# Optimization experiments

Hardware: AMD Instinct MI355X
Metric: run time of the kernel (lower is better)

The kernel has to match this reference:

```python
import jax, jax.numpy as jnp
import numpy as np

N_NODES = 50000


def _sage_conv(x, src, dst, Wl, Wr, bl, num_nodes):
    # PyG SAGEConv (mean aggr): out = lin_l(mean_{j in N(i)} x_j) + lin_r(x_i)
    # messages flow src -> dst
    agg = jax.ops.segment_sum(x[src], dst, num_segments=num_nodes)          # [N, F]
    deg = jax.ops.segment_sum(jnp.ones_like(dst, dtype=x.dtype), dst,
                              num_segments=num_nodes)                       # [N]
    agg = agg / jnp.maximum(deg, 1.0)[:, None]
    return agg @ Wl + bl + x @ Wr


def setup_inputs() -> dict:
    key = jax.random.key(0)
    ks = jax.random.split(key, 9)
    F_in, H, C, E = 256, 256, 40, 800000
    s = lambda fan: 1.0 / np.sqrt(fan)
    x = jax.random.normal(ks[0], (N_NODES, F_in), dtype=jnp.float32)
    edge_index = jax.random.randint(ks[1], (2, E), 0, N_NODES, dtype=jnp.int32)
    W1l = jax.random.normal(ks[2], (F_in, H), dtype=jnp.float32) * s(F_in)
    W1r = jax.random.normal(ks[3], (F_in, H), dtype=jnp.float32) * s(F_in)
    b1 = jnp.zeros((H,), dtype=jnp.float32)
    W2l = jax.random.normal(ks[4], (H, C), dtype=jnp.float32) * s(H)
    W2r = jax.random.normal(ks[5], (H, C), dtype=jnp.float32) * s(H)
    b2 = jnp.zeros((C,), dtype=jnp.float32)
    Q = jax.random.normal(ks[6], (E // 2, C), dtype=jnp.float32) * s(E // 2)
    return {"x": x, "edge_index": edge_index, "W1l": W1l, "b1": b1,
            "W1r": W1r, "W2l": W2l, "b2": b2, "W2r": W2r, "Q": Q}


def reference(x, edge_index, W1l, b1, W1r, W2l, b2, W2r, Q):
    # Eval mode: F.dropout with training=False is identity.
    src, dst = edge_index[0], edge_index[1]
    h = _sage_conv(x, src, dst, W1l, W1r, b1, N_NODES)
    h = jax.nn.elu(h)
    out = _sage_conv(h, src, dst, W2l, W2r, b2, N_NODES)
    return (out, Q)
```

## Files before the change

kernel.cpp:

```cpp
#include <hip/hip_runtime.h>
#include <hip/hip_bf16.h>
#include <cstddef>

#define N_NODES 50000
#define M_PAD 50048

typedef __attribute__((ext_vector_type(8))) short short8;
typedef __attribute__((ext_vector_type(4))) float floatx4;

__device__ inline unsigned short f2bf(float f) {
    union { float f; unsigned u; } v; v.f = f;
    unsigned r = v.u + 0x7fff + ((v.u >> 16) & 1);
    return (unsigned short)(r >> 16);
}
__device__ inline float bf2f(unsigned short s) {
    union { unsigned u; float f; } v; v.u = ((unsigned)s) << 16; return v.f;
}
__device__ inline float bfbits_lo(unsigned u) {
    union { unsigned u; float f; } v; v.u = u << 16; return v.f;
}
__device__ inline float bfbits_hi(unsigned u) {
    union { unsigned u; float f; } v; v.u = u & 0xffff0000u; return v.f;
}

__device__ inline void gload16(const void* g, void* l) {
    __builtin_amdgcn_global_load_lds(
        (const __attribute__((address_space(1))) unsigned int*)g,
        (__attribute__((address_space(3))) unsigned int*)l, 16, 0, 0);
}


__global__ void count_kernel(const int* __restrict__ dst, int* __restrict__ deg, int E) {
    for (int e = blockIdx.x * blockDim.x + threadIdx.x; e < E; e += gridDim.x * blockDim.x)
        atomicAdd(&deg[dst[e]], 1);
}

__global__ __launch_bounds__(256) void scan1_kernel(const int* __restrict__ deg,
                                                    int* __restrict__ blocksums, int n) {
    __shared__ int s[256];
    int t = threadIdx.x;
    int i = blockIdx.x * 256 + t;
    s[t] = (i < n) ? deg[i] : 0;
    __syncthreads();
    for (int off = 128; off > 0; off >>= 1) {
        if (t < off) s[t] += s[t + off];
        __syncthreads();
    }
    if (t == 0) blocksums[blockIdx.x] = s[0];
}

__global__ __launch_bounds__(256) void scan2_kernel(const int* __restrict__ blocksums,
                                                    int* __restrict__ blockoff, int nb) {
    __shared__ int s[256];
    int t = threadIdx.x;
    s[t] = (t < nb) ? blocksums[t] : 0;
    __syncthreads();
    for (int off = 1; off < 256; off <<= 1) {
        int u = (t >= off) ? s[t - off] : 0;
        __syncthreads();
        s[t] += u;
        __syncthreads();
    }
    if (t < nb) blockoff[t] = (t == 0) ? 0 : s[t - 1];
}

__global__ __launch_bounds__(256) void scan3_kernel(const int* __restrict__ deg,
                                                    const int* __restrict__ blockoff,
                                                    int* __restrict__ rowptr,
                                                    float* __restrict__ inv_deg,
                                                    int n, int E) {
    __shared__ int s[256];
    int t = threadIdx.x;
    int i = blockIdx.x * 256 + t;
    int v = (i < n) ? deg[i] : 0;
    s[t] = v;
    __syncthreads();
    for (int off = 1; off < 256; off <<= 1) {
        int u = (t >= off) ? s[t - off] : 0;
        __syncthreads();
        s[t] += u;
        __syncthreads();
    }
    if (i < n) {
        rowptr[i] = s[t] - v + blockoff[blockIdx.x];
        inv_deg[i] = 1.0f / (float)(v > 1 ? v : 1);
    }
    if (blockIdx.x == 0 && t == 0) rowptr[n] = E;
}

__global__ void fill_kernel(const int* __restrict__ src, const int* __restrict__ dst,
                            const int* __restrict__ rowptr, int* __restrict__ cnt,
                            int* __restrict__ csr, int E) {
    for (int e = blockIdx.x * blockDim.x + threadIdx.x; e < E; e += gridDim.x * blockDim.x) {
        int d = dst[e];
        int p = rowptr[d] + atomicAdd(&cnt[d], 1);
        csr[p] = src[e];
    }
}

__global__ __launch_bounds__(256) void prep_kernel(
    const float* __restrict__ x,
    const float* __restrict__ W1l, const float* __restrict__ W1r,
    const float* __restrict__ W2l, const float* __restrict__ W2r,
    unsigned short* __restrict__ Abuf, unsigned short* __restrict__ B1t,
    unsigned short* __restrict__ B2t) {
    int b = blockIdx.x;
    int tid = threadIdx.x;
    if (b < 6250) {
        int i = b * 256 + tid;
        int row = i >> 5;
        int c8 = i & 31;
        const float4* xp = reinterpret_cast<const float4*>(x + (size_t)row * 256 + c8 * 8);
        float4 v0 = xp[0], v1 = xp[1];
        uint4 o;
        o.x = (unsigned)f2bf(v0.x) | ((unsigned)f2bf(v0.y) << 16);
        o.y = (unsigned)f2bf(v0.z) | ((unsigned)f2bf(v0.w) << 16);
        o.z = (unsigned)f2bf(v1.x) | ((unsigned)f2bf(v1.y) << 16);
        o.w = (unsigned)f2bf(v1.z) | ((unsigned)f2bf(v1.w) << 16);
        *reinterpret_cast<uint4*>(Abuf + (size_t)row * 512 + 256 + c8 * 8) = o;
    } else if (b < 6250 + 512) {
        int idx = (b - 6250) * 256 + tid;
        int n = idx >> 9, k = idx & 511;
        float v = (k < 256) ? W1l[(size_t)k * 256 + n] : W1r[(size_t)(k - 256) * 256 + n];
        B1t[(size_t)n * 512 + k] = f2bf(v);
    } else {
        int idx = (b - 6250 - 512) * 256 + tid;
        int n = idx >> 8, k = idx & 255;
        float v = (n < 40) ? W2l[(size_t)k * 40 + n] : W2r[(size_t)k * 40 + (n - 40)];
        B2t[(size_t)n * 256 + k] = f2bf(v);
    }
}

__global__ __launch_bounds__(256) void aggregate1_q(
    const unsigned short* __restrict__ Abuf, const int* __restrict__ rowptr,
    const int* __restrict__ csr, const float* __restrict__ inv_deg,
    unsigned short* __restrict__ AbufOut, int N, int nAggBlocks,
    const float4* __restrict__ Qsrc, float4* __restrict__ Qdst, int nQ4) {
    if ((int)blockIdx.x >= nAggBlocks) {
        int idx = (blockIdx.x - nAggBlocks) * 256 + threadIdx.x;
        int stride = (gridDim.x - nAggBlocks) * 256;
        for (int i = idx; i < nQ4; i += stride) Qdst[i] = Qsrc[i];
        return;
    }
    int wv = blockIdx.x * 4 + (threadIdx.x >> 6);
    int node = wv * 2 + ((threadIdx.x >> 5) & 1);
    if (node >= N) return;
    int lane = threadIdx.x & 31;
    float a0 = 0.f, a1 = 0.f, a2 = 0.f, a3 = 0.f;
    float a4 = 0.f, a5 = 0.f, a6 = 0.f, a7 = 0.f;
    int beg = rowptr[node], end = rowptr[node + 1];
    int k = beg;
    for (; k + 4 <= end; k += 4) {
        uint4 v[4];
        #pragma unroll
        for (int u = 0; u < 4; ++u) {
            int j = csr[k + u];
            v[u] = *reinterpret_cast<const uint4*>(Abuf + (size_t)j * 512 + 256 + lane * 8);
        }
        #pragma unroll
        for (int u = 0; u < 4; ++u) {
            a0 += bfbits_lo(v[u].x); a1 += bfbits_hi(v[u].x);
            a2 += bfbits_lo(v[u].y); a3 += bfbits_hi(v[u].y);
            a4 += bfbits_lo(v[u].z); a5 += bfbits_hi(v[u].z);
            a6 += bfbits_lo(v[u].w); a7 += bfbits_hi(v[u].w);
        }
    }
    for (; k < end; ++k) {
        int j = csr[k];
        uint4 v = *reinterpret_cast<const uint4*>(Abuf + (size_t)j * 512 + 256 + lane * 8);
        a0 += bfbits_lo(v.x); a1 += bfbits_hi(v.x);
        a2 += bfbits_lo(v.y); a3 += bfbits_hi(v.y);
        a4 += bfbits_lo(v.z); a5 += bfbits_hi(v.z);
        a6 += bfbits_lo(v.w); a7 += bfbits_hi(v.w);
    }
    float s = inv_deg[node];
    uint4 w;
    w.x = (unsigned)f2bf(a0 * s) | ((unsigned)f2bf(a1 * s) << 16);
    w.y = (unsigned)f2bf(a2 * s) | ((unsigned)f2bf(a3 * s) << 16);
    w.z = (unsigned)f2bf(a4 * s) | ((unsigned)f2bf(a5 * s) << 16);
    w.w = (unsigned)f2bf(a6 * s) | ((unsigned)f2bf(a7 * s) << 16);
    *reinterpret_cast<uint4*>(AbufOut + (size_t)node * 512 + lane * 8) = w;
}

__global__ __launch_bounds__(256) void gemm1_mfma(
    const unsigned short* __restrict__ Abuf,
    const unsigned short* __restrict__ B1t,
    const float* __restrict__ bias,
    unsigned short* __restrict__ H,
    int M) {
    __shared__ unsigned short As[2][64 * 64];
    __shared__ unsigned short Bs[2][128 * 64];
    int tid = threadIdx.x;
    int row0 = blockIdx.x * 64;
    int bn = blockIdx.y;
    int wid = tid >> 6, lane = tid & 63;
    int wm = (wid >> 1) * 32;
    int wn = (wid & 1) * 64;
    int fr = lane & 15, fq = lane >> 4;

    int lrow8 = lane >> 3;
    int gco = ((lane & 7) ^ lrow8) * 8;
    const unsigned short* gA0 = Abuf + (size_t)(row0 + wid * 16 + 0 + lrow8) * 512 + gco;
    const unsigned short* gA1 = Abuf + (size_t)(row0 + wid * 16 + 8 + lrow8) * 512 + gco;
    const unsigned short* gB0 = B1t + (size_t)(bn * 128 + wid * 32 + 0  + lrow8) * 512 + gco;
    const unsigned short* gB1 = B1t + (size_t)(bn * 128 + wid * 32 + 8  + lrow8) * 512 + gco;
    const unsigned short* gB2 = B1t + (size_t)(bn * 128 + wid * 32 + 16 + lrow8) * 512 + gco;
    const unsigned short* gB3 = B1t + (size_t)(bn * 128 + wid * 32 + 24 + lrow8) * 512 + gco;

    floatx4 acc[2][4] = {};

    #define STAGE(buf, k0)                                       \
        gload16(gA0 + (k0), &As[buf][(wid * 16 + 0) * 64]);      \
        gload16(gA1 + (k0), &As[buf][(wid * 16 + 8) * 64]);      \
        gload16(gB0 + (k0), &Bs[buf][(wid * 32 + 0) * 64]);      \
        gload16(gB1 + (k0), &Bs[buf][(wid * 32 + 8) * 64]);      \
        gload16(gB2 + (k0), &Bs[buf][(wid * 32 + 16) * 64]);     \
        gload16(gB3 + (k0), &Bs[buf][(wid * 32 + 24) * 64]);

    #define COMPUTE(buf)                                                                  \
        {                                                                                 \
            _Pragma("unroll")                                                             \
            for (int kc = 0; kc < 2; ++kc) {                                              \
                short8 af[2], bfr[4];                                                     \
                _Pragma("unroll")                                                         \
                for (int mi = 0; mi < 2; ++mi) {                                          \
                    int row = wm + mi * 16 + fr;                                          \
                    af[mi] = *reinterpret_cast<const short8*>(                            \
                        &As[buf][row * 64 + (((kc * 4 + fq) ^ (fr & 7)) * 8)]);           \
                }                                                                         \
                _Pragma("unroll")                                                         \
                for (int ni = 0; ni < 4; ++ni) {                                          \
                    int row = wn + ni * 16 + fr;                                          \
                    bfr[ni] = *reinterpret_cast<const short8*>(                           \
                        &Bs[buf][row * 64 + (((kc * 4 + fq) ^ (fr & 7)) * 8)]);           \
                }                                                                         \
                _Pragma("unroll")                                                         \
                for (int mi = 0; mi < 2; ++mi)                                            \
                    _Pragma("unroll")                                                     \
                    for (int ni = 0; ni < 4; ++ni)                                        \
                        acc[mi][ni] = __builtin_amdgcn_mfma_f32_16x16x32_bf16(            \
                            af[mi], bfr[ni], acc[mi][ni], 0, 0, 0);                       \
            }                                                                             \
        }

    STAGE(0, 0);
    __syncthreads();
    int cur = 0;
    #pragma unroll 1
    for (int t = 0; t < 7; ++t) {
        STAGE(cur ^ 1, (t + 1) * 64);
        COMPUTE(cur);
        __syncthreads();
        cur ^= 1;
    }
    COMPUTE(cur);
    #undef STAGE
    #undef COMPUTE

    #pragma unroll
    for (int ni = 0; ni < 4; ++ni) {
        int gcol = bn * 128 + wn + ni * 16 + fr;
        float bb = bias[gcol];
        #pragma unroll
        for (int mi = 0; mi < 2; ++mi) {
            #pragma unroll
            for (int r = 0; r < 4; ++r) {
                int grow = row0 + wm + mi * 16 + fq * 4 + r;
                float t = acc[mi][ni][r] + bb;
                t = (t > 0.f) ? t : expm1f(t);
                H[(size_t)grow * 256 + gcol] = f2bf(t);
            }
        }
    }
}

__global__ __launch_bounds__(256) void gemm2_mfma(
    const unsigned short* __restrict__ Hb,
    const unsigned short* __restrict__ B2t,
    const float* __restrict__ b2,
    unsigned short* __restrict__ Plb,
    float* __restrict__ Pr,
    int M) {
    __shared__ unsigned short Bsm[80 * 256];
    __shared__ unsigned short As[2][64 * 64];
    int tid = threadIdx.x;
    int row0 = blockIdx.x * 64;
    int wid = tid >> 6, lane = tid & 63;
    int wm = wid * 16;
    int fr = lane & 15, fq = lane >> 4;

    for (int c = tid; c < 2560; c += 256) {
        int n = c >> 5, ci = c & 31;
        short8 v = *reinterpret_cast<const short8*>(B2t + (size_t)n * 256 + ci * 8);
        *reinterpret_cast<short8*>(&Bsm[n * 256 + ((ci ^ (n & 7)) * 8)]) = v;
    }

    int lrow8 = lane >> 3;
    int gco = ((lane & 7) ^ lrow8) * 8;
    const unsigned short* gA0 = Hb + (size_t)(row0 + wid * 16 + 0 + lrow8) * 256 + gco;
    const unsigned short* gA1 = Hb + (size_t)(row0 + wid * 16 + 8 + lrow8) * 256 + gco;

    floatx4 acc[5] = {};

    #define STAGE2(buf, k0)                                      \
        gload16(gA0 + (k0), &As[buf][(wid * 16 + 0) * 64]);      \
        gload16(gA1 + (k0), &As[buf][(wid * 16 + 8) * 64]);

    #define COMPUTE2(buf, k0)                                                             \
        {                                                                                 \
            _Pragma("unroll")                                                             \
            for (int kc = 0; kc < 2; ++kc) {                                              \
                short8 af;                                                                \
                {                                                                         \
                    int row = wm + fr;                                                    \
                    af = *reinterpret_cast<const short8*>(                                \
                        &As[buf][row * 64 + (((kc * 4 + fq) ^ (fr & 7)) * 8)]);           \
                }                                                                         \
                _Pragma("unroll")                                                         \
                for (int ni = 0; ni < 5; ++ni) {                                          \
                    int n = ni * 16 + fr;                                                 \
                    int c = ((k0) >> 3) + kc * 4 + fq;                                    \
                    short8 bfr = *reinterpret_cast<const short8*>(                        \
                        &Bsm[n * 256 + ((c ^ (n & 7)) * 8)]);                             \
                    acc[ni] = __builtin_amdgcn_mfma_f32_16x16x32_bf16(                    \
                        af, bfr, acc[ni], 0, 0, 0);                                       \
                }                                                                         \
            }                                                                             \
        }

    STAGE2(0, 0);
    __syncthreads();
    int cur = 0;
    #pragma unroll 1
    for (int t = 0; t < 3; ++t) {
        STAGE2(cur ^ 1, (t + 1) * 64);
        COMPUTE2(cur, t * 64);
        __syncthreads();
        cur ^= 1;
    }
    COMPUTE2(cur, 192);
    #undef STAGE2
    #undef COMPUTE2

    #pragma unroll
    for (int r = 0; r < 4; ++r) {
        int grow = row0 + wm + fq * 4 + r;
        if (grow < M) {
            #pragma unroll
            for (int ni = 0; ni < 5; ++ni) {
                int col = ni * 16 + fr;
                float v = acc[ni][r];
                if (col < 40)
                    Plb[(size_t)grow * 40 + col] = f2bf(v);
                else
                    Pr[(size_t)grow * 40 + (col - 40)] = v + b2[col - 40];
            }
        }
    }
}

__global__ __launch_bounds__(256) void final_kernel(
    const unsigned short* __restrict__ Plb, const float* __restrict__ Pr,
    const int* __restrict__ rowptr, const int* __restrict__ csr,
    const float* __restrict__ inv_deg, float* __restrict__ out, int N) {
    int wv = blockIdx.x * 4 + (threadIdx.x >> 6);
    int node = wv * 2 + ((threadIdx.x >> 5) & 1);
    if (node >= N) return;
    int lane = threadIdx.x & 31;
    if (lane >= 20) return;
    float s0 = 0.f, s1 = 0.f;
    int beg = rowptr[node], end = rowptr[node + 1];
    int k = beg;
    for (; k + 4 <= end; k += 4) {
        unsigned v0 = *reinterpret_cast<const unsigned*>(Plb + (size_t)csr[k]     * 40 + lane * 2);
        unsigned v1 = *reinterpret_cast<const unsigned*>(Plb + (size_t)csr[k + 1] * 40 + lane * 2);
        unsigned v2 = *reinterpret_cast<const unsigned*>(Plb + (size_t)csr[k + 2] * 40 + lane * 2);
        unsigned v3 = *reinterpret_cast<const unsigned*>(Plb + (size_t)csr[k + 3] * 40 + lane * 2);
        s0 += bfbits_lo(v0) + bfbits_lo(v1) + bfbits_lo(v2) + bfbits_lo(v3);
        s1 += bfbits_hi(v0) + bfbits_hi(v1) + bfbits_hi(v2) + bfbits_hi(v3);
    }
    for (; k < end; ++k) {
        unsigned v = *reinterpret_cast<const unsigned*>(Plb + (size_t)csr[k] * 40 + lane * 2);
        s0 += bfbits_lo(v);
        s1 += bfbits_hi(v);
    }
    float inv = inv_deg[node];
    float2 pr = *reinterpret_cast<const float2*>(Pr + (size_t)node * 40 + lane * 2);
    float2 o;
    o.x = s0 * inv + pr.x;
    o.y = s1 * inv + pr.y;
    *reinterpret_cast<float2*>(out + (size_t)node * 40 + lane * 2) = o;
}


extern "C" void kernel_launch(void* const* d_in, const int* in_sizes, int n_in,
                              void* d_out, int out_size, void* d_ws, size_t ws_size,
                              hipStream_t stream) {
    const float* x   = (const float*)d_in[0];
    const int*   ei  = (const int*)d_in[1];
    const float* W1l = (const float*)d_in[2];
    const float* b1  = (const float*)d_in[3];
    const float* W1r = (const float*)d_in[4];
    const float* W2l = (const float*)d_in[5];
    const float* b2  = (const float*)d_in[6];
    const float* W2r = (const float*)d_in[7];
    const float* Q   = (const float*)d_in[8];
    const int E = in_sizes[1] / 2;
    const int N = N_NODES;
    const int* src = ei;
    const int* dst = ei + E;
    const int NB = (N + 255) / 256;

    unsigned short* Abuf = (unsigned short*)d_ws;
    unsigned short* h    = Abuf + (size_t)M_PAD * 512;
    unsigned short* B1t  = h + (size_t)M_PAD * 256;
    unsigned short* B2t  = B1t + 256 * 512;
    unsigned short* Plb  = B2t + 80 * 256;
    float* Pr      = (float*)(Plb + (size_t)N * 40 + 32);
    float* inv_deg = Pr + (size_t)N * 40;
    int*   deg     = (int*)(inv_deg + N);
    int*   cnt     = deg + N;
    int*   rowptr  = cnt + N;
    int*   blocksums = rowptr + N + 1;
    int*   blockoff  = blocksums + NB;
    int*   csr     = blockoff + NB;

    float* out = (float*)d_out;

    hipMemsetAsync(deg, 0, sizeof(int) * 2 * (size_t)N, stream);
    count_kernel<<<1024, 256, 0, stream>>>(dst, deg, E);
    scan1_kernel<<<NB, 256, 0, stream>>>(deg, blocksums, N);
    scan2_kernel<<<1, 256, 0, stream>>>(blocksums, blockoff, NB);
    scan3_kernel<<<NB, 256, 0, stream>>>(deg, blockoff, rowptr, inv_deg, N, E);
    fill_kernel<<<1024, 256, 0, stream>>>(src, dst, rowptr, cnt, csr, E);

    prep_kernel<<<6250 + 512 + 80, 256, 0, stream>>>(x, W1l, W1r, W2l, W2r,
                                                     Abuf, B1t, B2t);

    const int nAggBlocks = (N + 7) / 8;
    const int nQ4 = in_sizes[8] / 4;
    aggregate1_q<<<nAggBlocks + 2048, 256, 0, stream>>>(
        Abuf, rowptr, csr, inv_deg, Abuf, N, nAggBlocks,
        (const float4*)Q, (float4*)(out + (size_t)N * 40), nQ4);

    gemm1_mfma<<<dim3(M_PAD / 64, 2), 256, 0, stream>>>(Abuf, B1t, b1, h, N);
    gemm2_mfma<<<M_PAD / 64, 256, 0, stream>>>(h, B2t, b2, Plb, Pr, N);
    final_kernel<<<(N + 7) / 8, 256, 0, stream>>>(Plb, Pr, rowptr, csr, inv_deg, out, N);
}
```

Measured before the change: 259.6 us.

## Fuse degree count into prep, Q copy into fill, one node per wave in aggregate

Merges the edge degree-count atomics into the prep (bf16 conversion/transpose) kernel and moves the Q passthrough copy into the CSR fill kernel, cutting the number of launches and letting independent work share a grid. The first-layer aggregation now gives each node a full 64-lane wave, with the two half-waves taking alternating edges and combining partial sums through a cross-lane shuffle. This raises memory-level parallelism per node but doubles the number of waves and adds shuffle reductions.

```diff
diff --git a/kernel.cpp b/kernel.cpp
--- a/kernel.cpp
+++ b/kernel.cpp
@@ -13,9 +13,6 @@
     unsigned r = v.u + 0x7fff + ((v.u >> 16) & 1);
     return (unsigned short)(r >> 16);
 }
-__device__ inline float bf2f(unsigned short s) {
-    union { unsigned u; float f; } v; v.u = ((unsigned)s) << 16; return v.f;
-}
 __device__ inline float bfbits_lo(unsigned u) {
     union { unsigned u; float f; } v; v.u = u << 16; return v.f;
 }
@@ -29,81 +26,13 @@
         (__attribute__((address_space(3))) unsigned int*)l, 16, 0, 0);
 }
 
-
-__global__ void count_kernel(const int* __restrict__ dst, int* __restrict__ deg, int E) {
-    for (int e = blockIdx.x * blockDim.x + threadIdx.x; e < E; e += gridDim.x * blockDim.x)
-        atomicAdd(&deg[dst[e]], 1);
-}
-
-__global__ __launch_bounds__(256) void scan1_kernel(const int* __restrict__ deg,
-                                                    int* __restrict__ blocksums, int n) {
-    __shared__ int s[256];
-    int t = threadIdx.x;
-    int i = blockIdx.x * 256 + t;
-    s[t] = (i < n) ? deg[i] : 0;
-    __syncthreads();
-    for (int off = 128; off > 0; off >>= 1) {
-        if (t < off) s[t] += s[t + off];
-        __syncthreads();
-    }
-    if (t == 0) blocksums[blockIdx.x] = s[0];
-}
-
-__global__ __launch_bounds__(256) void scan2_kernel(const int* __restrict__ blocksums,
-                                                    int* __restrict__ blockoff, int nb) {
-    __shared__ int s[256];
-    int t = threadIdx.x;
-    s[t] = (t < nb) ? blocksums[t] : 0;
-    __syncthreads();
-    for (int off = 1; off < 256; off <<= 1) {
-        int u = (t >= off) ? s[t - off] : 0;
-        __syncthreads();
-        s[t] += u;
-        __syncthreads();
-    }
-    if (t < nb) blockoff[t] = (t == 0) ? 0 : s[t - 1];
-}
-
-__global__ __launch_bounds__(256) void scan3_kernel(const int* __restrict__ deg,
-                                                    const int* __restrict__ blockoff,
-                                                    int* __restrict__ rowptr,
-                                                    float* __restrict__ inv_deg,
-                                                    int n, int E) {
-    __shared__ int s[256];
-    int t = threadIdx.x;
-    int i = blockIdx.x * 256 + t;
-    int v = (i < n) ? deg[i] : 0;
-    s[t] = v;
-    __syncthreads();
-    for (int off = 1; off < 256; off <<= 1) {
-        int u = (t >= off) ? s[t - off] : 0;
-        __syncthreads();
-        s[t] += u;
-        __syncthreads();
-    }
-    if (i < n) {
-        rowptr[i] = s[t] - v + blockoff[blockIdx.x];
-        inv_deg[i] = 1.0f / (float)(v > 1 ? v : 1);
-    }
-    if (blockIdx.x == 0 && t == 0) rowptr[n] = E;
-}
-
-__global__ void fill_kernel(const int* __restrict__ src, const int* __restrict__ dst,
-                            const int* __restrict__ rowptr, int* __restrict__ cnt,
-                            int* __restrict__ csr, int E) {
-    for (int e = blockIdx.x * blockDim.x + threadIdx.x; e < E; e += gridDim.x * blockDim.x) {
-        int d = dst[e];
-        int p = rowptr[d] + atomicAdd(&cnt[d], 1);
-        csr[p] = src[e];
-    }
-}
-
-__global__ __launch_bounds__(256) void prep_kernel(
+__global__ __launch_bounds__(256) void prep_count(
     const float* __restrict__ x,
     const float* __restrict__ W1l, const float* __restrict__ W1r,
     const float* __restrict__ W2l, const float* __restrict__ W2r,
     unsigned short* __restrict__ Abuf, unsigned short* __restrict__ B1t,
-    unsigned short* __restrict__ B2t) {
+    unsigned short* __restrict__ B2t,
+    const int* __restrict__ dst, int* __restrict__ deg, int E) {
     int b = blockIdx.x;
     int tid = threadIdx.x;
     if (b < 6250) {
@@ -123,63 +52,136 @@
         int n = idx >> 9, k = idx & 511;
         float v = (k < 256) ? W1l[(size_t)k * 256 + n] : W1r[(size_t)(k - 256) * 256 + n];
         B1t[(size_t)n * 512 + k] = f2bf(v);
-    } else {
-        int idx = (b - 6250 - 512) * 256 + tid;
+    } else if (b < 6842) {
+        int idx = (b - 6762) * 256 + tid;
         int n = idx >> 8, k = idx & 255;
         float v = (n < 40) ? W2l[(size_t)k * 40 + n] : W2r[(size_t)k * 40 + (n - 40)];
         B2t[(size_t)n * 256 + k] = f2bf(v);
-    }
-}
-
-__global__ __launch_bounds__(256) void aggregate1_q(
+    } else {
+        int base = (b - 6842) * 256 + tid;
+        for (int e = base; e < E; e += 1024 * 256)
+            atomicAdd(&deg[dst[e]], 1);
+    }
+}
+
+__global__ __launch_bounds__(256) void scan1_kernel(const int* __restrict__ deg,
+                                                    int* __restrict__ blocksums, int n) {
+    __shared__ int s[256];
+    int t = threadIdx.x;
+    int i = blockIdx.x * 256 + t;
+    s[t] = (i < n) ? deg[i] : 0;
+    __syncthreads();
+    for (int off = 128; off > 0; off >>= 1) {
+        if (t < off) s[t] += s[t + off];
+        __syncthreads();
+    }
+    if (t == 0) blocksums[blockIdx.x] = s[0];
+}
+
+__global__ __launch_bounds__(256) void scan2_kernel(const int* __restrict__ blocksums,
+                                                    int* __restrict__ blockoff, int nb) {
+    __shared__ int s[256];
+    int t = threadIdx.x;
+    s[t] = (t < nb) ? blocksums[t] : 0;
+    __syncthreads();
+    for (int off = 1; off < 256; off <<= 1) {
+        int u = (t >= off) ? s[t - off] : 0;
+        __syncthreads();
+        s[t] += u;
+        __syncthreads();
+    }
+    if (t < nb) blockoff[t] = (t == 0) ? 0 : s[t - 1];
+}
+
+__global__ __launch_bounds__(256) void scan3_kernel(const int* __restrict__ deg,
+                                                    const int* __restrict__ blockoff,
+                                                    int* __restrict__ rowptr,
+                                                    float* __restrict__ inv_deg,
+                                                    int n, int E) {
+    __shared__ int s[256];
+    int t = threadIdx.x;
+    int i = blockIdx.x * 256 + t;
+    int v = (i < n) ? deg[i] : 0;
+    s[t] = v;
+    __syncthreads();
+    for (int off = 1; off < 256; off <<= 1) {
+        int u = (t >= off) ? s[t - off] : 0;
+        __syncthreads();
+        s[t] += u;
+        __syncthreads();
+    }
+    if (i < n) {
+        rowptr[i] = s[t] - v + blockoff[blockIdx.x];
+        inv_deg[i] = 1.0f / (float)(v > 1 ? v : 1);
+    }
+    if (blockIdx.x == 0 && t == 0) rowptr[n] = E;
+}
+
+__global__ void fill_q(const int* __restrict__ src, const int* __restrict__ dst,
+                       const int* __restrict__ rowptr, int* __restrict__ cnt,
+                       int* __restrict__ csr, int E,
+                       const float4* __restrict__ Qsrc, float4* __restrict__ Qdst,
+                       int nQ4) {
+    if ((int)blockIdx.x >= 1024) {
+        int idx = (blockIdx.x - 1024) * 256 + threadIdx.x;
+        for (int i = idx; i < nQ4; i += 1024 * 256) Qdst[i] = Qsrc[i];
+        return;
+    }
+    for (int e = blockIdx.x * blockDim.x + threadIdx.x; e < E; e += 1024 * 256) {
+        int d = dst[e];
+        int p = rowptr[d] + atomicAdd(&cnt[d], 1);
+        csr[p] = src[e];
+    }
+}
+
+__global__ __launch_bounds__(256) void aggregate1(
     const unsigned short* __restrict__ Abuf, const int* __restrict__ rowptr,
     const int* __restrict__ csr, const float* __restrict__ inv_deg,
-    unsigned short* __restrict__ AbufOut, int N, int nAggBlocks,
-    const float4* __restrict__ Qsrc, float4* __restrict__ Qdst, int nQ4) {
-    if ((int)blockIdx.x >= nAggBlocks) {
-        int idx = (blockIdx.x - nAggBlocks) * 256 + threadIdx.x;
-        int stride = (gridDim.x - nAggBlocks) * 256;
-        for (int i = idx; i < nQ4; i += stride) Qdst[i] = Qsrc[i];
-        return;
-    }
-    int wv = blockIdx.x * 4 + (threadIdx.x >> 6);
-    int node = wv * 2 + ((threadIdx.x >> 5) & 1);
+    unsigned short* __restrict__ AbufOut, int N) {
+    int node = blockIdx.x * 4 + (threadIdx.x >> 6);
     if (node >= N) return;
-    int lane = threadIdx.x & 31;
+    int lane = threadIdx.x & 63;
+    int half = lane >> 5;
+    int dlane = lane & 31;
+    const unsigned short* base = Abuf + 256 + (size_t)dlane * 8;
     float a0 = 0.f, a1 = 0.f, a2 = 0.f, a3 = 0.f;
     float a4 = 0.f, a5 = 0.f, a6 = 0.f, a7 = 0.f;
     int beg = rowptr[node], end = rowptr[node + 1];
-    int k = beg;
-    for (; k + 4 <= end; k += 4) {
-        uint4 v[4];
-        #pragma unroll
-        for (int u = 0; u < 4; ++u) {
-            int j = csr[k + u];
-            v[u] = *reinterpret_cast<const uint4*>(Abuf + (size_t)j * 512 + 256 + lane * 8);
-        }
-        #pragma unroll
-        for (int u = 0; u < 4; ++u) {
-            a0 += bfbits_lo(v[u].x); a1 += bfbits_hi(v[u].x);
-            a2 += bfbits_lo(v[u].y); a3 += bfbits_hi(v[u].y);
-            a4 += bfbits_lo(v[u].z); a5 += bfbits_hi(v[u].z);
-            a6 += bfbits_lo(v[u].w); a7 += bfbits_hi(v[u].w);
-        }
-    }
-    for (; k < end; ++k) {
+    int k = beg + half;
+    for (; k + 7 < end; k += 8) {
+        int j0 = csr[k], j1 = csr[k + 2], j2 = csr[k + 4], j3 = csr[k + 6];
+        uint4 v0 = *reinterpret_cast<const uint4*>(base + (size_t)j0 * 512);
+        uint4 v1 = *reinterpret_cast<const uint4*>(base + (size_t)j1 * 512);
+        uint4 v2 = *reinterpret_cast<const uint4*>(base + (size_t)j2 * 512);
+        uint4 v3 = *reinterpret_cast<const uint4*>(base + (size_t)j3 * 512);
+        a0 += bfbits_lo(v0.x); a1 += bfbits_hi(v0.x); a2 += bfbits_lo(v0.y); a3 += bfbits_hi(v0.y);
+        a4 += bfbits_lo(v0.z); a5 += bfbits_hi(v0.z); a6 += bfbits_lo(v0.w); a7 += bfbits_hi(v0.w);
+        a0 += bfbits_lo(v1.x); a1 += bfbits_hi(v1.x); a2 += bfbits_lo(v1.y); a3 += bfbits_hi(v1.y);
+        a4 += bfbits_lo(v1.z); a5 += bfbits_hi(v1.z); a6 += bfbits_lo(v1.w); a7 += bfbits_hi(v1.w);
+        a0 += bfbits_lo(v2.x); a1 += bfbits_hi(v2.x); a2 += bfbits_lo(v2.y); a3 += bfbits_hi(v2.y);
+        a4 += bfbits_lo(v2.z); a5 += bfbits_hi(v2.z); a6 += bfbits_lo(v2.w); a7 += bfbits_hi(v2.w);
+        a0 += bfbits_lo(v3.x); a1 += bfbits_hi(v3.x); a2 += bfbits_lo(v3.y); a3 += bfbits_hi(v3.y);
+        a4 += bfbits_lo(v3.z); a5 += bfbits_hi(v3.z); a6 += bfbits_lo(v3.w); a7 += bfbits_hi(v3.w);
+    }
+    for (; k < end; k += 2) {
         int j = csr[k];
-        uint4 v = *reinterpret_cast<const uint4*>(Abuf + (size_t)j * 512 + 256 + lane * 8);
-        a0 += bfbits_lo(v.x); a1 += bfbits_hi(v.x);
-        a2 += bfbits_lo(v.y); a3 += bfbits_hi(v.y);
-        a4 += bfbits_lo(v.z); a5 += bfbits_hi(v.z);
-        a6 += bfbits_lo(v.w); a7 += bfbits_hi(v.w);
-    }
-    float s = inv_deg[node];
-    uint4 w;
-    w.x = (unsigned)f2bf(a0 * s) | ((unsigned)f2bf(a1 * s) << 16);
-    w.y = (unsigned)f2bf(a2 * s) | ((unsigned)f2bf(a3 * s) << 16);
-    w.z = (unsigned)f2bf(a4 * s) | ((unsigned)f2bf(a5 * s) << 16);
-    w.w = (unsigned)f2bf(a6 * s) | ((unsigned)f2bf(a7 * s) << 16);
-    *reinterpret_cast<uint4*>(AbufOut + (size_t)node * 512 + lane * 8) = w;
+        uint4 v = *reinterpret_cast<const uint4*>(base + (size_t)j * 512);
+        a0 += bfbits_lo(v.x); a1 += bfbits_hi(v.x); a2 += bfbits_lo(v.y); a3 += bfbits_hi(v.y);
+        a4 += bfbits_lo(v.z); a5 += bfbits_hi(v.z); a6 += bfbits_lo(v.w); a7 += bfbits_hi(v.w);
+    }
+    a0 += __shfl_xor(a0, 32, 64); a1 += __shfl_xor(a1, 32, 64);
+    a2 += __shfl_xor(a2, 32, 64); a3 += __shfl_xor(a3, 32, 64);
+    a4 += __shfl_xor(a4, 32, 64); a5 += __shfl_xor(a5, 32, 64);
+    a6 += __shfl_xor(a6, 32, 64); a7 += __shfl_xor(a7, 32, 64);
+    if (half == 0) {
+        float s = inv_deg[node];
+        uint4 w;
+        w.x = (unsigned)f2bf(a0 * s) | ((unsigned)f2bf(a1 * s) << 16);
+        w.y = (unsigned)f2bf(a2 * s) | ((unsigned)f2bf(a3 * s) << 16);
+        w.z = (unsigned)f2bf(a4 * s) | ((unsigned)f2bf(a5 * s) << 16);
+        w.w = (unsigned)f2bf(a6 * s) | ((unsigned)f2bf(a7 * s) << 16);
+        *reinterpret_cast<uint4*>(AbufOut + (size_t)node * 512 + dlane * 8) = w;
+    }
 }
 
 __global__ __launch_bounds__(256) void gemm1_mfma(
@@ -428,21 +430,18 @@
     float* out = (float*)d_out;
 
     hipMemsetAsync(deg, 0, sizeof(int) * 2 * (size_t)N, stream);
-    count_kernel<<<1024, 256, 0, stream>>>(dst, deg, E);
+    prep_count<<<6842 + 1024, 256, 0, stream>>>(x, W1l, W1r, W2l, W2r,
+                                                Abuf, B1t, B2t, dst, deg, E);
     scan1_kernel<<<NB, 256, 0, stream>>>(deg, blocksums, N);
     scan2_kernel<<<1, 256, 0, stream>>>(blocksums, blockoff, NB);
     scan3_kernel<<<NB, 256, 0, stream>>>(deg, blockoff, rowptr, inv_deg, N, E);
-    fill_kernel<<<1024, 256, 0, stream>>>(src, dst, rowptr, cnt, csr, E);
-
-    prep_kernel<<<6250 + 512 + 80, 256, 0, stream>>>(x, W1l, W1r, W2l, W2r,
-                                                     Abuf, B1t, B2t);
-
-    const int nAggBlocks = (N + 7) / 8;
+
     const int nQ4 = in_sizes[8] / 4;
-    aggregate1_q<<<nAggBlocks + 2048, 256, 0, stream>>>(
-        Abuf, rowptr, csr, inv_deg, Abuf, N, nAggBlocks,
-        (const float4*)Q, (float4*)(out + (size_t)N * 40), nQ4);
-
+    fill_q<<<2048, 256, 0, stream>>>(src, dst, rowptr, cnt, csr, E,
+                                     (const float4*)Q,
+                                     (float4*)(out + (size_t)N * 40), nQ4);
+
+    aggregate1<<<(N + 3) / 4, 256, 0, stream>>>(Abuf, rowptr, csr, inv_deg, Abuf, N);
     gemm1_mfma<<<dim3(M_PAD / 64, 2), 256, 0, stream>>>(Abuf, B1t, b1, h, N);
     gemm2_mfma<<<M_PAD / 64, 256, 0, stream>>>(h, B2t, b2, Plb, Pr, N);
     final_kernel<<<(N + 7) / 8, 256, 0, stream>>>(Plb, Pr, rowptr, csr, inv_deg, out, N);
```

Result: no change. 255.7 us (-1.5%).
